# Optimization experiments

Measured on AMD Instinct MI355X. Metric: run time of the kernel, lower is better.

Reference implementation:

```python
import jax, jax.numpy as jnp
import numpy as np

B, T, C = 8, 2048, 512
H = 8
DH = C // H
MLP = 4 * C
EPS = 1e-5


def _ln(x, w, b):
    m = jnp.mean(x, axis=-1, keepdims=True)
    v = jnp.mean(jnp.square(x - m), axis=-1, keepdims=True)
    return (x - m) * jax.lax.rsqrt(v + EPS) * w + b


def setup_inputs() -> dict:
    key = jax.random.key(0)
    ks = jax.random.split(key, 12)
    s = 0.02
    return {
        "x": jax.random.normal(ks[0], (B, T, C), jnp.float32),
        "c": jax.random.normal(ks[1], (B, C), jnp.float32),
        "qkv_w": jax.random.normal(ks[2], (3 * C, C), jnp.float32) * s,
        "qkv_b": jnp.zeros((3 * C,), jnp.float32),
        "proj_w": jax.random.normal(ks[3], (C, C), jnp.float32) * s,
        "proj_b": jnp.zeros((C,), jnp.float32),
        "ada_w": jax.random.normal(ks[4], (6 * C, C), jnp.float32) * s,
        "ada_b": jnp.zeros((6 * C,), jnp.float32),
        "fc1_w": jax.random.normal(ks[5], (MLP, C), jnp.float32) * s,
        "fc1_b": jnp.zeros((MLP,), jnp.float32),
        "fc2_w": jax.random.normal(ks[6], (C, MLP), jnp.float32) * s,
        "fc2_b": jnp.zeros((C,), jnp.float32),
        "ln1_w": jnp.ones((C,), jnp.float32),
        "ln1_b": jnp.zeros((C,), jnp.float32),
        "ln2_w": jnp.ones((C,), jnp.float32),
        "ln2_b": jnp.zeros((C,), jnp.float32),
    }


def reference(x, c, qkv_w, qkv_b, proj_w, proj_b, ada_w, ada_b,
              fc1_w, fc1_b, fc2_w, fc2_b, ln1_w, ln1_b, ln2_w, ln2_b):
    # AdaLN modulation: SiLU -> Linear -> chunk into 6 [B,C] pieces
    mod = jax.nn.silu(c) @ ada_w.T + ada_b  # [B, 6C]
    sh_msa, sc_msa, g_msa, sh_mlp, sc_mlp, g_mlp = jnp.split(mod, 6, axis=1)

    # --- attention branch ---
    h = _ln(x, ln1_w, ln1_b) * (1.0 + sc_msa[:, None, :]) + sh_msa[:, None, :]
    qkv = h @ qkv_w.T + qkv_b  # [B, T, 3C]
    q, k, v = jnp.split(qkv, 3, axis=-1)
    q = q.reshape(B, T, H, DH).transpose(0, 2, 1, 3)  # [B,H,T,Dh]
    k = k.reshape(B, T, H, DH).transpose(0, 2, 1, 3)
    v = v.reshape(B, T, H, DH).transpose(0, 2, 1, 3)
    scores = jnp.einsum('bhqd,bhkd->bhqk', q, k) * (1.0 / np.sqrt(DH))
    w = jax.nn.softmax(scores, axis=-1)
    o = jnp.einsum('bhqk,bhkd->bhqd', w, v)  # [B,H,T,Dh]
    o = o.transpose(0, 2, 1, 3).reshape(B, T, C)
    attn = o @ proj_w.T + proj_b
    x = x + g_msa[:, None, :] * attn

    # --- MLP branch ---
    h2 = _ln(x, ln2_w, ln2_b) * (1.0 + sc_mlp[:, None, :]) + sh_mlp[:, None, :]
    m = jax.nn.gelu(h2 @ fc1_w.T + fc1_b, approximate=True) @ fc2_w.T + fc2_b
    return x + g_mlp[:, None, :] * m
```

## Files before the change

kernel.cpp:

```cpp
#include <hip/hip_runtime.h>
#include <cstdint>
#include <cstddef>

typedef unsigned short u16;
typedef short v8s __attribute__((ext_vector_type(8)));
typedef float v4f __attribute__((ext_vector_type(4)));
typedef float f32x16 __attribute__((ext_vector_type(16)));
typedef unsigned int v4u __attribute__((ext_vector_type(4)));
typedef unsigned short v4u16 __attribute__((ext_vector_type(4)));

#define TT 2048
#define CC 512

#define QSCALE 0.18033688011112042f

__device__ __forceinline__ u16 f2bf(float f) {
    unsigned u = __float_as_uint(f);
    u += 0x7fffu + ((u >> 16) & 1u);
    return (u16)(u >> 16);
}

__device__ __forceinline__ unsigned cvt_pk_bf16(float lo, float hi) {
    unsigned r;
    asm("v_cvt_pk_bf16_f32 %0, %1, %2" : "=v"(r) : "v"(lo), "v"(hi));
    return r;
}

__device__ __forceinline__ void swap32(unsigned a, unsigned b, unsigned& x, unsigned& y) {
#if __has_builtin(__builtin_amdgcn_permlane32_swap)
    auto r = __builtin_amdgcn_permlane32_swap(a, b, false, false);
    x = r[0]; y = r[1];
#else
    unsigned bx = (unsigned)__shfl_xor((int)b, 32, 64);
    unsigned ax = (unsigned)__shfl_xor((int)a, 32, 64);
    bool hi5 = (threadIdx.x & 32) != 0;
    x = hi5 ? bx : a;
    y = hi5 ? b : ax;
#endif
}

__device__ __forceinline__ void gl2lds16(const void* g, void* l) {
    __builtin_amdgcn_global_load_lds(
        (const __attribute__((address_space(1))) unsigned int*)g,
        (__attribute__((address_space(3))) unsigned int*)l,
        16, 0, 0);
}

__global__ __launch_bounds__(256) void f2bf_all(const float* __restrict__ s0,
                                                const float* __restrict__ s1,
                                                const float* __restrict__ s2,
                                                const float* __restrict__ s3,
                                                u16* __restrict__ d) {
    int i = (blockIdx.x * 256 + threadIdx.x) * 4;
    const float* s; int off;
    if (i < 786432)       { s = s0; off = 0; }
    else if (i < 1048576) { s = s1; off = 786432; }
    else if (i < 2097152) { s = s2; off = 1048576; }
    else                  { s = s3; off = 2097152; }
    float4 v = *(const float4*)(s + (i - off));
    v4u16 r;
    r[0] = f2bf(v.x); r[1] = f2bf(v.y); r[2] = f2bf(v.z); r[3] = f2bf(v.w);
    *(v4u16*)(d + i) = r;
}

__global__ __launch_bounds__(256) void ada_kernel(const float* __restrict__ c,
                                                  const float* __restrict__ W,
                                                  const float* __restrict__ bias,
                                                  float* __restrict__ mod) {
    int idx = blockIdx.x * 4 + (threadIdx.x >> 6);
    int l = threadIdx.x & 63;
    int bb = idx / 3072;
    int n = idx - bb * 3072;
    const float* cp = c + bb * CC;
    const float* wp = W + (size_t)n * CC;
    float s = 0.f;
    #pragma unroll
    for (int i = 0; i < 8; ++i) {
        int k = l * 8 + i;
        float cv = cp[k];
        float sil = cv / (1.f + __expf(-cv));
        s += sil * wp[k];
    }
    #pragma unroll
    for (int off = 32; off; off >>= 1) s += __shfl_xor(s, off, 64);
    if (l == 0) mod[idx] = s + bias[n];
}

__global__ __launch_bounds__(256) void ln_mod_kernel(const float* __restrict__ X,
                                                     const float* __restrict__ lnw,
                                                     const float* __restrict__ lnb,
                                                     const float* __restrict__ mod,
                                                     int sh_off, int sc_off,
                                                     u16* __restrict__ out) {
    int row = blockIdx.x * 4 + (threadIdx.x >> 6);
    int l = threadIdx.x & 63;
    int b = row >> 11;
    const float* xr = X + (size_t)row * CC + l * 8;
    float4 va = *(const float4*)(xr);
    float4 vb = *(const float4*)(xr + 4);
    float v[8] = {va.x, va.y, va.z, va.w, vb.x, vb.y, vb.z, vb.w};
    float s = 0.f;
    #pragma unroll
    for (int i = 0; i < 8; ++i) s += v[i];
    #pragma unroll
    for (int off = 32; off; off >>= 1) s += __shfl_xor(s, off, 64);
    float mean = s * (1.f / CC);
    float q = 0.f;
    #pragma unroll
    for (int i = 0; i < 8; ++i) { float d = v[i] - mean; q += d * d; }
    #pragma unroll
    for (int off = 32; off; off >>= 1) q += __shfl_xor(q, off, 64);
    float rstd = rsqrtf(q * (1.f / CC) + 1e-5f);
    int col = l * 8;
    const float* shp = mod + b * 3072 + sh_off + col;
    const float* scp = mod + b * 3072 + sc_off + col;
    v8s st;
    #pragma unroll
    for (int i = 0; i < 8; ++i) {
        float hv = (v[i] - mean) * rstd * lnw[col + i] + lnb[col + i];
        float r = hv * (1.f + scp[i]) + shp[i];
        st[i] = (short)f2bf(r);
    }
    *(v8s*)(out + (size_t)row * CC + col) = st;
}

__global__ __launch_bounds__(512) void vt_kernel(const u16* __restrict__ qkv,
                                                 u16* __restrict__ vT) {
    __shared__ u16 tile[64 * 72];
    const int id = blockIdx.x;
    const int bh = id >> 5, tt = id & 31;
    const int b = bh >> 3, h = bh & 7;
    const int tid = threadIdx.x;
    const int tr = tid >> 3, d0 = (tid & 7) * 8;
    v8s v = *(const v8s*)(qkv + (size_t)(b * TT + tt * 64 + tr) * 1536 + 1024 + h * 64 + d0);
    *(v8s*)(&tile[tr * 72 + d0]) = v;
    __syncthreads();
    const int dr = tid >> 3, t0 = (tid & 7) * 8;
    v8s ov;
    #pragma unroll
    for (int e = 0; e < 8; ++e) ov[e] = (short)tile[(t0 + e) * 72 + dr];
    *(v8s*)(vT + (size_t)(bh * 64 + dr) * TT + tt * 64 + t0) = ov;
}

template <int MODE>
__global__ __launch_bounds__(256)
void gemm_bt(const u16* __restrict__ A, const u16* __restrict__ W,
             const float* __restrict__ bias, void* __restrict__ outp,
             const float* __restrict__ resid, const float* __restrict__ gate,
             int NX, int N, int K) {
    __shared__ alignas(16) u16 Al[2][4096];
    __shared__ alignas(16) u16 Bl[2][4096];
    const int id = blockIdx.x;
    const int wg = (id & 7) * (gridDim.x >> 3) + (id >> 3);
    const int by = wg / NX, bx = wg - by * NX;
    const int bn = bx << 7, bm = by << 7;
    const int tid = threadIdx.x;
    const int w = tid >> 6, l = tid & 63;
    const int hi = l >> 4, lo = l & 15;
    const int wr = (w >> 1) << 6, wc = (w & 1) << 6;

    v4f acc[4][4] = {};

    const int srow = l >> 2;
    const int sp = l & 3;
    const int NT = K >> 5;

    auto stage = [&](int buf, int kt) {
        const int k0 = kt << 5;
        #pragma unroll
        for (int i = 0; i < 2; ++i) {
            const int c = w + (i << 2);
            const int row = (c << 4) + srow;
            const int lg = sp ^ ((row >> 1) & 3);
            gl2lds16(A + (size_t)(bm + row) * K + k0 + (lg << 3), &Al[buf][c << 9]);
            gl2lds16(W + (size_t)(bn + row) * K + k0 + (lg << 3), &Bl[buf][c << 9]);
        }
    };

    stage(0, 0);
    __syncthreads();
    int cur = 0;
    for (int t = 0; t < NT; ++t) {
        if (t + 1 < NT) stage(cur ^ 1, t + 1);
        const u16* Ab = Al[cur];
        const u16* Bb = Bl[cur];
        v8s aF[4], bF[4];
        #pragma unroll
        for (int mi = 0; mi < 4; ++mi) {
            int r = wr + (mi << 4) + lo;
            aF[mi] = *(const v8s*)(Ab + (r << 5) + ((hi ^ ((r >> 1) & 3)) << 3));
        }
        #pragma unroll
        for (int ni = 0; ni < 4; ++ni) {
            int r = wc + (ni << 4) + lo;
            bF[ni] = *(const v8s*)(Bb + (r << 5) + ((hi ^ ((r >> 1) & 3)) << 3));
        }
        #pragma unroll
        for (int mi = 0; mi < 4; ++mi)
            #pragma unroll
            for (int ni = 0; ni < 4; ++ni)
                acc[mi][ni] = __builtin_amdgcn_mfma_f32_16x16x32_bf16(
                    aF[mi], bF[ni], acc[mi][ni], 0, 0, 0);
        __syncthreads();
        cur ^= 1;
    }

    #pragma unroll
    for (int mi = 0; mi < 4; ++mi) {
        #pragma unroll
        for (int ni = 0; ni < 4; ++ni) {
            int col = bn + wc + (ni << 4) + lo;
            float bv = bias[col];
            #pragma unroll
            for (int j = 0; j < 4; ++j) {
                int row = bm + wr + (mi << 4) + hi * 4 + j;
                float v = acc[mi][ni][j] + bv;
                if constexpr (MODE == 0) {
                    float sc2 = (col < 512) ? QSCALE : 1.0f;
                    ((u16*)outp)[(size_t)row * N + col] = f2bf(v * sc2);
                } else if constexpr (MODE == 1) {
                    float u2 = 1.5957691216057308f * (v + 0.044715f * v * v * v);
                    float g = v / (1.f + __expf(-u2));
                    ((u16*)outp)[(size_t)row * N + col] = f2bf(g);
                } else {
                    float r = resid[(size_t)row * N + col];
                    float gt = gate[(row >> 11) * 3072 + col];
                    ((float*)outp)[(size_t)row * N + col] = r + gt * v;
                }
            }
        }
    }
}

__global__ __launch_bounds__(512, 4)
void attn_kernel(const u16* __restrict__ qkv, const u16* __restrict__ vT,
                 u16* __restrict__ O) {
    __shared__ alignas(16) u16 smem[18432];
    const int tid = threadIdx.x;
    const int w = tid >> 6, l = tid & 63;
    const int l31 = l & 31, l5 = l >> 5;
    const int id = blockIdx.x;
    const int bh = id & 63, b = bh >> 3, h = bh & 7;
    const int qt = id >> 6;

    const int qrow = qt * 256 + w * 32 + l31;
    const u16* qp = qkv + (size_t)(b * TT + qrow) * 1536 + h * 64;
    v8s qf[4];
    #pragma unroll
    for (int ks = 0; ks < 4; ++ks) qf[ks] = *(const v8s*)(qp + ks * 16 + l5 * 8);

    const int r8 = l >> 3;
    const int kc = (l & 7) ^ r8 ^ w;
    const u16* kptr = qkv + (size_t)(b * TT + 8 * w + r8) * 1536 + 512 + h * 64 + kc * 8;
    const u16* vptr = vT + (size_t)(bh * 64 + 8 * w + r8) * TT + kc * 8;

    auto stageKV = [&](int it, int buf) {
        gl2lds16(kptr + (size_t)it * 64 * 1536, smem + buf * 4096 + w * 512);
        gl2lds16(vptr + it * 64, smem + 8192 + buf * 4096 + w * 512);
    };

    const char* sbase = (const char*)smem;
    int offs[8];
    #pragma unroll
    for (int t = 0; t < 2; ++t)
        #pragma unroll
        for (int ks = 0; ks < 4; ++ks) {
            int row = t * 32 + l31;
            int phys = ((ks << 1) + l5) ^ (row & 7) ^ ((row >> 3) & 7);
            offs[t * 4 + ks] = row * 128 + phys * 16;
        }

    v8s onesf;
    #pragma unroll
    for (int i = 0; i < 8; ++i) onesf[i] = (short)0x3F80;

    stageKV(0, 0);
    __syncthreads();

    f32x16 o[2] = {};
    f32x16 lacc = {};

    #pragma unroll 2
    for (int it = 0; it < 32; ++it) {
        const int cur = it & 1;
        if (it + 1 < 32) stageKV(it + 1, cur ^ 1);
        const int koff = cur * 8192;

        f32x16 st[2];
        st[0] = (f32x16)0.f; st[1] = (f32x16)0.f;
        __builtin_amdgcn_s_setprio(1);
        #pragma unroll
        for (int ks = 0; ks < 4; ++ks) {
            v8s k0 = *(const v8s*)(sbase + offs[ks] + koff);
            v8s k1 = *(const v8s*)(sbase + offs[4 + ks] + koff);
            st[0] = __builtin_amdgcn_mfma_f32_32x32x16_bf16(k0, qf[ks], st[0], 0, 0, 0);
            st[1] = __builtin_amdgcn_mfma_f32_32x32x16_bf16(k1, qf[ks], st[1], 0, 0, 0);
        }
        __builtin_amdgcn_s_setprio(0);

        #pragma unroll
        for (int t2 = 0; t2 < 2; ++t2)
            #pragma unroll
            for (int r = 0; r < 16; ++r)
                st[t2][r] = __builtin_exp2f(st[t2][r]);

        __builtin_amdgcn_s_setprio(1);
        #pragma unroll
        for (int ks = 0; ks < 4; ++ks) {
            const int tt = ks >> 1, rb = (ks & 1) * 8;
            unsigned pkA = cvt_pk_bf16(st[tt][rb + 0], st[tt][rb + 1]);
            unsigned pkB = cvt_pk_bf16(st[tt][rb + 4], st[tt][rb + 5]);
            unsigned pkC = cvt_pk_bf16(st[tt][rb + 2], st[tt][rb + 3]);
            unsigned pkD = cvt_pk_bf16(st[tt][rb + 6], st[tt][rb + 7]);
            unsigned w0, w1, w2, w3;
            swap32(pkA, pkB, w0, w2);
            swap32(pkC, pkD, w1, w3);
            v4u pw; pw[0] = w0; pw[1] = w1; pw[2] = w2; pw[3] = w3;
            v8s pa = __builtin_bit_cast(v8s, pw);
            v8s vf0 = *(const v8s*)(sbase + offs[ks] + koff + 16384);
            v8s vf1 = *(const v8s*)(sbase + offs[4 + ks] + koff + 16384);
            o[0] = __builtin_amdgcn_mfma_f32_32x32x16_bf16(vf0, pa, o[0], 0, 0, 0);
            o[1] = __builtin_amdgcn_mfma_f32_32x32x16_bf16(vf1, pa, o[1], 0, 0, 0);
            lacc = __builtin_amdgcn_mfma_f32_32x32x16_bf16(onesf, pa, lacc, 0, 0, 0);
        }
        __builtin_amdgcn_s_setprio(0);
        __syncthreads();
    }

    float inv = 1.f / lacc[0];
    char* outw = (char*)smem + w * 4608;
    #pragma unroll
    for (int t2 = 0; t2 < 2; ++t2)
        #pragma unroll
        for (int r = 0; r < 16; r += 2) {
            int dh = t2 * 32 + (r & 3) + ((r >> 2) << 3) + (l5 << 2);
            unsigned pk = cvt_pk_bf16(o[t2][r] * inv, o[t2][r + 1] * inv);
            *(unsigned*)(outw + l31 * 144 + dh * 2) = pk;
        }
    __syncthreads();
    #pragma unroll
    for (int i = 0; i < 4; ++i) {
        int idx = (i << 9) + tid;
        int qq = idx >> 3, cch = idx & 7;
        v8s vd = *(const v8s*)((char*)smem + (qq >> 5) * 4608 + (qq & 31) * 144 + cch * 16);
        *(v8s*)(O + (size_t)(b * TT + qt * 256 + qq) * 512 + h * 64 + cch * 8) = vd;
    }
}

extern "C" void kernel_launch(void* const* d_in, const int* in_sizes, int n_in,
                              void* d_out, int out_size, void* d_ws, size_t ws_size,
                              hipStream_t stream) {
    const float* x = (const float*)d_in[0];
    const float* c = (const float*)d_in[1];
    const float* qkv_w = (const float*)d_in[2];
    const float* qkv_b = (const float*)d_in[3];
    const float* proj_w = (const float*)d_in[4];
    const float* proj_b = (const float*)d_in[5];
    const float* ada_w = (const float*)d_in[6];
    const float* ada_b = (const float*)d_in[7];
    const float* fc1_w = (const float*)d_in[8];
    const float* fc1_b = (const float*)d_in[9];
    const float* fc2_w = (const float*)d_in[10];
    const float* fc2_b = (const float*)d_in[11];
    const float* ln1_w = (const float*)d_in[12];
    const float* ln1_b = (const float*)d_in[13];
    const float* ln2_w = (const float*)d_in[14];
    const float* ln2_b = (const float*)d_in[15];

    char* p = (char*)d_ws;
    auto carve = [&](size_t bytes) -> char* {
        char* r = p;
        p += (bytes + 255) & ~(size_t)255;
        return r;
    };
    float* mod  = (float*)carve((size_t)8 * 3072 * 4);
    u16* hbuf   = (u16*)carve((size_t)16384 * 512 * 2);
    u16* qkvb   = (u16*)carve((size_t)16384 * 1536 * 2);
    u16* attno  = (u16*)carve((size_t)16384 * 512 * 2);
    float* x1   = (float*)carve((size_t)16384 * 512 * 4);
    u16* wall   = (u16*)carve((size_t)3145728 * 2);
    u16* wq  = wall;
    u16* wpj = wall + 786432;
    u16* w1  = wall + 1048576;
    u16* w2  = wall + 2097152;
    u16* fc1g = qkvb;
    u16* vT   = hbuf;

    f2bf_all<<<3072, 256, 0, stream>>>(qkv_w, proj_w, fc1_w, fc2_w, wall);

    ada_kernel<<<24576 / 4, 256, 0, stream>>>(c, ada_w, ada_b, mod);

    ln_mod_kernel<<<16384 / 4, 256, 0, stream>>>(x, ln1_w, ln1_b, mod, 0, 512, hbuf);
    gemm_bt<0><<<12 * 128, 256, 0, stream>>>(hbuf, wq, qkv_b, qkvb,
                                             nullptr, nullptr, 12, 1536, 512);
    vt_kernel<<<64 * 32, 512, 0, stream>>>(qkvb, vT);
    attn_kernel<<<512, 512, 0, stream>>>(qkvb, vT, attno);
    gemm_bt<2><<<4 * 128, 256, 0, stream>>>(attno, wpj, proj_b, x1,
                                            x, mod + 2 * 512, 4, 512, 512);

    ln_mod_kernel<<<16384 / 4, 256, 0, stream>>>(x1, ln2_w, ln2_b, mod, 3 * 512, 4 * 512, hbuf);
    gemm_bt<1><<<16 * 128, 256, 0, stream>>>(hbuf, w1, fc1_b, fc1g,
                                             nullptr, nullptr, 16, 2048, 512);
    gemm_bt<2><<<4 * 128, 256, 0, stream>>>(fc1g, w2, fc2_b, (float*)d_out,
                                            x1, mod + 5 * 512, 4, 512, 2048);
}
```

Before: 321.7 us.

## Split attention key tiles across wave halves and double the attention grid

Each attention block now covers 128 query rows instead of 256, so the grid doubles from 512 to 1024 blocks. Within a block, the two groups of four waves each handle half of every 64-key tile. Their partial outputs and row sums are combined through shared memory, with the second half's partial output passed as bf16. The hardware exp2 is also replaced by a floor-plus-cubic-polynomial approximation. This aims to raise occupancy and lower per-wave latency, at the cost of an extra LDS reduction, each K/V tile being loaded by twice as many blocks, and some extra rounding error.

```diff
diff --git a/kernel.cpp b/kernel.cpp
--- a/kernel.cpp
+++ b/kernel.cpp
@@ -7,6 +7,7 @@
 typedef float v4f __attribute__((ext_vector_type(4)));
 typedef float f32x16 __attribute__((ext_vector_type(16)));
 typedef unsigned int v4u __attribute__((ext_vector_type(4)));
+typedef unsigned int v2u __attribute__((ext_vector_type(2)));
 typedef unsigned short v4u16 __attribute__((ext_vector_type(4)));
 
 #define TT 2048
@@ -20,10 +21,25 @@
     return (u16)(u >> 16);
 }
 
+__device__ __forceinline__ float bf2f(u16 v) {
+    return __uint_as_float(((unsigned)v) << 16);
+}
+
 __device__ __forceinline__ unsigned cvt_pk_bf16(float lo, float hi) {
     unsigned r;
     asm("v_cvt_pk_bf16_f32 %0, %1, %2" : "=v"(r) : "v"(lo), "v"(hi));
     return r;
+}
+
+__device__ __forceinline__ float fexp2(float x) {
+    float xf = __builtin_floorf(x);
+    float f = x - xf;
+    float p = __builtin_fmaf(f,
+              __builtin_fmaf(f,
+              __builtin_fmaf(f, 0.0781455737f, 0.2261731467f),
+                                0.6955568569f), 1.0f);
+    int e = (int)xf;
+    return __uint_as_float(__float_as_uint(p) + ((unsigned)(e << 23)));
 }
 
 __device__ __forceinline__ void swap32(unsigned a, unsigned b, unsigned& x, unsigned& y) {
@@ -236,14 +252,17 @@
 void attn_kernel(const u16* __restrict__ qkv, const u16* __restrict__ vT,
                  u16* __restrict__ O) {
     __shared__ alignas(16) u16 smem[18432];
+    char* const sb = (char*)smem;
     const int tid = threadIdx.x;
     const int w = tid >> 6, l = tid & 63;
     const int l31 = l & 31, l5 = l >> 5;
+    const int p = w & 3;
+    const int half = w >> 2;
     const int id = blockIdx.x;
     const int bh = id & 63, b = bh >> 3, h = bh & 7;
     const int qt = id >> 6;
 
-    const int qrow = qt * 256 + w * 32 + l31;
+    const int qrow = qt * 128 + p * 32 + l31;
     const u16* qp = qkv + (size_t)(b * TT + qrow) * 1536 + h * 64;
     v8s qf[4];
     #pragma unroll
@@ -259,7 +278,6 @@
         gl2lds16(vptr + it * 64, smem + 8192 + buf * 4096 + w * 512);
     };
 
-    const char* sbase = (const char*)smem;
     int offs[8];
     #pragma unroll
     for (int t = 0; t < 2; ++t)
@@ -286,39 +304,35 @@
         if (it + 1 < 32) stageKV(it + 1, cur ^ 1);
         const int koff = cur * 8192;
 
-        f32x16 st[2];
-        st[0] = (f32x16)0.f; st[1] = (f32x16)0.f;
+        f32x16 st = (f32x16)0.f;
         __builtin_amdgcn_s_setprio(1);
         #pragma unroll
         for (int ks = 0; ks < 4; ++ks) {
-            v8s k0 = *(const v8s*)(sbase + offs[ks] + koff);
-            v8s k1 = *(const v8s*)(sbase + offs[4 + ks] + koff);
-            st[0] = __builtin_amdgcn_mfma_f32_32x32x16_bf16(k0, qf[ks], st[0], 0, 0, 0);
-            st[1] = __builtin_amdgcn_mfma_f32_32x32x16_bf16(k1, qf[ks], st[1], 0, 0, 0);
+            v8s k0 = *(const v8s*)(sb + offs[half * 4 + ks] + koff);
+            st = __builtin_amdgcn_mfma_f32_32x32x16_bf16(k0, qf[ks], st, 0, 0, 0);
         }
         __builtin_amdgcn_s_setprio(0);
 
         #pragma unroll
-        for (int t2 = 0; t2 < 2; ++t2)
-            #pragma unroll
-            for (int r = 0; r < 16; ++r)
-                st[t2][r] = __builtin_exp2f(st[t2][r]);
+        for (int r = 0; r < 16; ++r)
+            st[r] = fexp2(st[r]);
 
         __builtin_amdgcn_s_setprio(1);
         #pragma unroll
-        for (int ks = 0; ks < 4; ++ks) {
-            const int tt = ks >> 1, rb = (ks & 1) * 8;
-            unsigned pkA = cvt_pk_bf16(st[tt][rb + 0], st[tt][rb + 1]);
-            unsigned pkB = cvt_pk_bf16(st[tt][rb + 4], st[tt][rb + 5]);
-            unsigned pkC = cvt_pk_bf16(st[tt][rb + 2], st[tt][rb + 3]);
-            unsigned pkD = cvt_pk_bf16(st[tt][rb + 6], st[tt][rb + 7]);
+        for (int ks2 = 0; ks2 < 2; ++ks2) {
+            const int rb = ks2 * 8;
+            unsigned pkA = cvt_pk_bf16(st[rb + 0], st[rb + 1]);
+            unsigned pkB = cvt_pk_bf16(st[rb + 4], st[rb + 5]);
+            unsigned pkC = cvt_pk_bf16(st[rb + 2], st[rb + 3]);
+            unsigned pkD = cvt_pk_bf16(st[rb + 6], st[rb + 7]);
             unsigned w0, w1, w2, w3;
             swap32(pkA, pkB, w0, w2);
             swap32(pkC, pkD, w1, w3);
             v4u pw; pw[0] = w0; pw[1] = w1; pw[2] = w2; pw[3] = w3;
             v8s pa = __builtin_bit_cast(v8s, pw);
-            v8s vf0 = *(const v8s*)(sbase + offs[ks] + koff + 16384);
-            v8s vf1 = *(const v8s*)(sbase + offs[4 + ks] + koff + 16384);
+            const int slot = half * 2 + ks2;
+            v8s vf0 = *(const v8s*)(sb + offs[slot] + koff + 16384);
+            v8s vf1 = *(const v8s*)(sb + offs[4 + slot] + koff + 16384);
             o[0] = __builtin_amdgcn_mfma_f32_32x32x16_bf16(vf0, pa, o[0], 0, 0, 0);
             o[1] = __builtin_amdgcn_mfma_f32_32x32x16_bf16(vf1, pa, o[1], 0, 0, 0);
             lacc = __builtin_amdgcn_mfma_f32_32x32x16_bf16(onesf, pa, lacc, 0, 0, 0);
@@ -327,23 +341,51 @@
         __syncthreads();
     }
 
-    float inv = 1.f / lacc[0];
-    char* outw = (char*)smem + w * 4608;
-    #pragma unroll
-    for (int t2 = 0; t2 < 2; ++t2)
-        #pragma unroll
-        for (int r = 0; r < 16; r += 2) {
-            int dh = t2 * 32 + (r & 3) + ((r >> 2) << 3) + (l5 << 2);
-            unsigned pk = cvt_pk_bf16(o[t2][r] * inv, o[t2][r + 1] * inv);
-            *(unsigned*)(outw + l31 * 144 + dh * 2) = pk;
-        }
+    const int PB = 18944;
+    if (half) {
+        #pragma unroll
+        for (int dt = 0; dt < 2; ++dt)
+            #pragma unroll
+            for (int jj = 0; jj < 4; ++jj) {
+                v2u pk;
+                pk[0] = cvt_pk_bf16(o[dt][4 * jj + 0], o[dt][4 * jj + 1]);
+                pk[1] = cvt_pk_bf16(o[dt][4 * jj + 2], o[dt][4 * jj + 3]);
+                *(v2u*)(sb + PB + p * 4096 + (dt * 4 + jj) * 512 + l * 8) = pk;
+            }
+        if (l5 == 0)
+            *(float*)(sb + 35328 + p * 256 + l31 * 4) = lacc[0];
+    }
     __syncthreads();
-    #pragma unroll
-    for (int i = 0; i < 4; ++i) {
+    if (!half) {
+        float lsum = lacc[0] + *(const float*)(sb + 35328 + p * 256 + l31 * 4);
+        float inv = 1.f / lsum;
+        #pragma unroll
+        for (int dt = 0; dt < 2; ++dt)
+            #pragma unroll
+            for (int jj = 0; jj < 4; ++jj) {
+                v2u rd = *(const v2u*)(sb + PB + p * 4096 + (dt * 4 + jj) * 512 + l * 8);
+                o[dt][4 * jj + 0] += bf2f((u16)(rd[0] & 0xffffu));
+                o[dt][4 * jj + 1] += bf2f((u16)(rd[0] >> 16));
+                o[dt][4 * jj + 2] += bf2f((u16)(rd[1] & 0xffffu));
+                o[dt][4 * jj + 3] += bf2f((u16)(rd[1] >> 16));
+            }
+        char* outw = sb + p * 4608;
+        #pragma unroll
+        for (int t2 = 0; t2 < 2; ++t2)
+            #pragma unroll
+            for (int r = 0; r < 16; r += 2) {
+                int dh = t2 * 32 + (r & 3) + ((r >> 2) << 3) + (l5 << 2);
+                unsigned pk = cvt_pk_bf16(o[t2][r] * inv, o[t2][r + 1] * inv);
+                *(unsigned*)(outw + l31 * 144 + dh * 2) = pk;
+            }
+    }
+    __syncthreads();
+    #pragma unroll
+    for (int i = 0; i < 2; ++i) {
         int idx = (i << 9) + tid;
         int qq = idx >> 3, cch = idx & 7;
-        v8s vd = *(const v8s*)((char*)smem + (qq >> 5) * 4608 + (qq & 31) * 144 + cch * 16);
-        *(v8s*)(O + (size_t)(b * TT + qt * 256 + qq) * 512 + h * 64 + cch * 8) = vd;
+        v8s vd = *(const v8s*)(sb + (qq >> 5) * 4608 + (qq & 31) * 144 + cch * 16);
+        *(v8s*)(O + (size_t)(b * TT + qt * 128 + qq) * 512 + h * 64 + cch * 8) = vd;
     }
 }
 
@@ -394,7 +436,7 @@
     gemm_bt<0><<<12 * 128, 256, 0, stream>>>(hbuf, wq, qkv_b, qkvb,
                                              nullptr, nullptr, 12, 1536, 512);
     vt_kernel<<<64 * 32, 512, 0, stream>>>(qkvb, vT);
-    attn_kernel<<<512, 512, 0, stream>>>(qkvb, vT, attno);
+    attn_kernel<<<1024, 512, 0, stream>>>(qkvb, vT, attno);
     gemm_bt<2><<<4 * 128, 256, 0, stream>>>(attno, wpj, proj_b, x1,
                                             x, mod + 2 * 512, 4, 512, 512);
 
```

Result: no change. 327.6 us (+1.9%).
